# Optimization experiments

Hardware: AMD Instinct MI355X
Metric: run time of the kernel (lower is better)

The kernel has to match this reference:

```python
import jax, jax.numpy as jnp
import numpy as np

T, B = 8192, 4096  # n_time_steps, n_seqs


def setup_inputs() -> dict:
    key = jax.random.key(0)
    k1, k2 = jax.random.split(key)
    # Binary Bernoulli(0.5) observations, shape (T, B, 1), as the delta rule expects
    x = jnp.round(jax.random.uniform(k1, (T, B, 1), dtype=jnp.float32))
    # log-uniform learning rate per init_parameters: lr = 10 ** U(-2.5, -0.5)
    lr = 10.0 ** jax.random.uniform(k2, (), jnp.float32, minval=-2.5, maxval=-0.5)
    return {"x": x, "lr": lr}


def reference(x, lr):
    # DeltaRule forward, order=1 ('transition' / bigram) branch.
    # Gated EMA recurrence over time:
    #   p0_t = p0_{t-1} + lr * (x_t - p0_{t-1}) * (1 - x_{t-1})
    #   p1_t = p1_{t-1} + lr * (x_t - p1_{t-1}) * x_{t-1}
    # prediction_t = p0_t * (1 - x_t) + p1_t * x_t
    eff_lr = jnp.clip(lr, 0.0, 1.0)  # torch .clamp(0,1)
    obs = x[:, :, 0]  # (T, B)
    n_seqs = obs.shape[1]
    half = jnp.full((n_seqs,), 0.5, dtype=obs.dtype)
    init = (half, half, jnp.zeros((n_seqs,), dtype=obs.dtype))  # p0, p1, obs_prev

    def step(carry, x_t):
        p0, p1, obs_prev = carry
        p0 = p0 + eff_lr * (x_t - p0) * (1.0 - obs_prev)
        p1 = p1 + eff_lr * (x_t - p1) * obs_prev
        pred = p0 * (1.0 - x_t) + p1 * x_t
        return (p0, p1, x_t), pred

    _, preds = jax.lax.scan(step, init, obs)  # preds: (T, B)
    return preds[:, :, None]  # (T, B, 1), matching unsqueeze(2)
```

## Files before the change

kernel.cpp:

```cpp
#include <hip/hip_runtime.h>


constexpr int T_LEN  = 8192;
constexpr int B_SEQ  = 4096;
constexpr int B4     = B_SEQ / 4;
constexpr int CHUNK  = 64;
constexpr int NCHUNK = T_LEN / CHUNK;
constexpr int BLOCK  = 256;

__device__ __forceinline__ float clamp01(float v) {
    return fminf(fmaxf(v, 0.0f), 1.0f);
}

__global__ __launch_bounds__(BLOCK) void p1_compose(
    const float4* __restrict__ x4, const float* __restrict__ lr_ptr,
    float4* __restrict__ cA0, float4* __restrict__ cB0,
    float4* __restrict__ cA1, float4* __restrict__ cB1)
{
    const int i  = blockIdx.x * BLOCK + threadIdx.x;
    const int c  = blockIdx.y;
    const int t0 = c * CHUNK;
    const float lr = clamp01(*lr_ptr);

    float obs[4];
    float A0[4] = {1.f,1.f,1.f,1.f}, Bc0[4] = {0.f,0.f,0.f,0.f};
    float A1[4] = {1.f,1.f,1.f,1.f}, Bc1[4] = {0.f,0.f,0.f,0.f};

    if (c == 0) {
        obs[0]=obs[1]=obs[2]=obs[3]=0.f;
    } else {
        float4 o = x4[(size_t)(t0 - 1) * B4 + i];
        obs[0]=o.x; obs[1]=o.y; obs[2]=o.z; obs[3]=o.w;
    }

    for (int t = t0; t < t0 + CHUNK; ++t) {
        float4 xv = x4[(size_t)t * B4 + i];
        float xt[4] = {xv.x, xv.y, xv.z, xv.w};
        #pragma unroll
        for (int k = 0; k < 4; ++k) {
            float g  = 1.0f - obs[k];
            float l0 = lr * g;
            float l1 = lr * obs[k];
            float a0 = 1.0f - l0;
            float a1 = 1.0f - l1;
            A0[k] *= a0;  Bc0[k] = fmaf(a0, Bc0[k], l0 * xt[k]);
            A1[k] *= a1;  Bc1[k] = fmaf(a1, Bc1[k], l1 * xt[k]);
            obs[k] = xt[k];
        }
    }

    const size_t idx = (size_t)c * B4 + i;
    cA0[idx] = make_float4(A0[0], A0[1], A0[2], A0[3]);
    cB0[idx] = make_float4(Bc0[0], Bc0[1], Bc0[2], Bc0[3]);
    cA1[idx] = make_float4(A1[0], A1[1], A1[2], A1[3]);
    cB1[idx] = make_float4(Bc1[0], Bc1[1], Bc1[2], Bc1[3]);
}

__global__ __launch_bounds__(BLOCK) void p2_scan(
    const float4* __restrict__ cA0, const float4* __restrict__ cB0,
    const float4* __restrict__ cA1, const float4* __restrict__ cB1,
    float4* __restrict__ sP0, float4* __restrict__ sP1)
{
    const int i = blockIdx.x * BLOCK + threadIdx.x;
    float p0[4] = {0.5f,0.5f,0.5f,0.5f};
    float p1[4] = {0.5f,0.5f,0.5f,0.5f};

    for (int c = 0; c < NCHUNK; ++c) {
        const size_t idx = (size_t)c * B4 + i;
        sP0[idx] = make_float4(p0[0], p0[1], p0[2], p0[3]);
        sP1[idx] = make_float4(p1[0], p1[1], p1[2], p1[3]);
        float4 a0 = cA0[idx], b0 = cB0[idx];
        float4 a1 = cA1[idx], b1 = cB1[idx];
        p0[0] = fmaf(a0.x, p0[0], b0.x);
        p0[1] = fmaf(a0.y, p0[1], b0.y);
        p0[2] = fmaf(a0.z, p0[2], b0.z);
        p0[3] = fmaf(a0.w, p0[3], b0.w);
        p1[0] = fmaf(a1.x, p1[0], b1.x);
        p1[1] = fmaf(a1.y, p1[1], b1.y);
        p1[2] = fmaf(a1.z, p1[2], b1.z);
        p1[3] = fmaf(a1.w, p1[3], b1.w);
    }
}

__global__ __launch_bounds__(BLOCK) void p3_emit(
    const float4* __restrict__ x4, const float* __restrict__ lr_ptr,
    const float4* __restrict__ sP0, const float4* __restrict__ sP1,
    float4* __restrict__ out4)
{
    const int i  = blockIdx.x * BLOCK + threadIdx.x;
    const int c  = blockIdx.y;
    const int t0 = c * CHUNK;
    const float lr = clamp01(*lr_ptr);

    const size_t sidx = (size_t)c * B4 + i;
    float4 P0 = sP0[sidx], P1 = sP1[sidx];
    float p0[4] = {P0.x, P0.y, P0.z, P0.w};
    float p1[4] = {P1.x, P1.y, P1.z, P1.w};

    float obs[4];
    if (c == 0) {
        obs[0]=obs[1]=obs[2]=obs[3]=0.f;
    } else {
        float4 o = x4[(size_t)(t0 - 1) * B4 + i];
        obs[0]=o.x; obs[1]=o.y; obs[2]=o.z; obs[3]=o.w;
    }

    for (int t = t0; t < t0 + CHUNK; ++t) {
        float4 xv = x4[(size_t)t * B4 + i];
        float xt[4] = {xv.x, xv.y, xv.z, xv.w};
        float pr[4];
        #pragma unroll
        for (int k = 0; k < 4; ++k) {
            float g = 1.0f - obs[k];
            p0[k] = fmaf(lr * g,      xt[k] - p0[k], p0[k]);
            p1[k] = fmaf(lr * obs[k], xt[k] - p1[k], p1[k]);
            pr[k] = fmaf(p1[k] - p0[k], xt[k], p0[k]);
            obs[k] = xt[k];
        }
        out4[(size_t)t * B4 + i] = make_float4(pr[0], pr[1], pr[2], pr[3]);
    }
}

extern "C" void kernel_launch(void* const* d_in, const int* in_sizes, int n_in,
                              void* d_out, int out_size, void* d_ws, size_t ws_size,
                              hipStream_t stream) {
    const float4* x4  = (const float4*)d_in[0];
    const float*  lr  = (const float*)d_in[1];
    float4*       out = (float4*)d_out;

    const size_t n = (size_t)NCHUNK * B4;
    float4* cA0 = (float4*)d_ws;
    float4* cB0 = cA0 + n;
    float4* cA1 = cB0 + n;
    float4* cB1 = cA1 + n;
    float4* sP0 = cB1 + n;
    float4* sP1 = sP0 + n;

    dim3 grid(B4 / BLOCK, NCHUNK);
    p1_compose<<<grid, BLOCK, 0, stream>>>(x4, lr, cA0, cB0, cA1, cB1);
    p2_scan<<<dim3(B4 / BLOCK), BLOCK, 0, stream>>>(cA0, cB0, cA1, cB1, sP0, sP1);
    p3_emit<<<grid, BLOCK, 0, stream>>>(x4, lr, sP0, sP1, out);
}
```

Baseline: 302.9 us.

## Bit-pack observations in compose pass and parallelize chunk scan with wave shuffles

The compose pass now also packs each chunk's binary observations into 64-bit masks. The emit pass reads those masks instead of re-reading the full float input, which cuts its input traffic by about 32x. The serial chunk-carry scan is replaced by a parallel scan: one block per column group, 128 threads over chunks, shuffle-based within a wave plus a shared-memory fix-up across waves. This adds workspace writes for the bitmasks, depends on the inputs being exactly 0/1, and changes the floating-point association of the carry composition.

```diff
diff --git a/kernel.cpp b/kernel.cpp
--- a/kernel.cpp
+++ b/kernel.cpp
@@ -15,7 +15,8 @@
 __global__ __launch_bounds__(BLOCK) void p1_compose(
     const float4* __restrict__ x4, const float* __restrict__ lr_ptr,
     float4* __restrict__ cA0, float4* __restrict__ cB0,
-    float4* __restrict__ cA1, float4* __restrict__ cB1)
+    float4* __restrict__ cA1, float4* __restrict__ cB1,
+    uint4* __restrict__ bitsA, uint4* __restrict__ bitsB)
 {
     const int i  = blockIdx.x * BLOCK + threadIdx.x;
     const int c  = blockIdx.y;
@@ -23,9 +24,6 @@
     const float lr = clamp01(*lr_ptr);
 
     float obs[4];
-    float A0[4] = {1.f,1.f,1.f,1.f}, Bc0[4] = {0.f,0.f,0.f,0.f};
-    float A1[4] = {1.f,1.f,1.f,1.f}, Bc1[4] = {0.f,0.f,0.f,0.f};
-
     if (c == 0) {
         obs[0]=obs[1]=obs[2]=obs[3]=0.f;
     } else {
@@ -33,18 +31,24 @@
         obs[0]=o.x; obs[1]=o.y; obs[2]=o.z; obs[3]=o.w;
     }
 
-    for (int t = t0; t < t0 + CHUNK; ++t) {
-        float4 xv = x4[(size_t)t * B4 + i];
+    float A0[4]  = {1.f,1.f,1.f,1.f}, Bc0[4] = {0.f,0.f,0.f,0.f};
+    float A1[4]  = {1.f,1.f,1.f,1.f}, Bc1[4] = {0.f,0.f,0.f,0.f};
+    unsigned long long bits[4] = {0ull,0ull,0ull,0ull};
+
+    #pragma unroll 8
+    for (int t = 0; t < CHUNK; ++t) {
+        float4 xv = x4[(size_t)(t0 + t) * B4 + i];
         float xt[4] = {xv.x, xv.y, xv.z, xv.w};
         #pragma unroll
         for (int k = 0; k < 4; ++k) {
+            bits[k] |= ((unsigned long long)(xt[k] != 0.0f)) << t;
             float g  = 1.0f - obs[k];
             float l0 = lr * g;
-            float l1 = lr * obs[k];
+            float l1 = lr - l0;
             float a0 = 1.0f - l0;
             float a1 = 1.0f - l1;
-            A0[k] *= a0;  Bc0[k] = fmaf(a0, Bc0[k], l0 * xt[k]);
-            A1[k] *= a1;  Bc1[k] = fmaf(a1, Bc1[k], l1 * xt[k]);
+            Bc0[k] = fmaf(a0, Bc0[k], l0 * xt[k]);  A0[k] *= a0;
+            Bc1[k] = fmaf(a1, Bc1[k], l1 * xt[k]);  A1[k] *= a1;
             obs[k] = xt[k];
         }
     }
@@ -54,37 +58,81 @@
     cB0[idx] = make_float4(Bc0[0], Bc0[1], Bc0[2], Bc0[3]);
     cA1[idx] = make_float4(A1[0], A1[1], A1[2], A1[3]);
     cB1[idx] = make_float4(Bc1[0], Bc1[1], Bc1[2], Bc1[3]);
-}
-
-__global__ __launch_bounds__(BLOCK) void p2_scan(
+    bitsA[idx] = make_uint4((unsigned)bits[0], (unsigned)(bits[0] >> 32),
+                            (unsigned)bits[1], (unsigned)(bits[1] >> 32));
+    bitsB[idx] = make_uint4((unsigned)bits[2], (unsigned)(bits[2] >> 32),
+                            (unsigned)bits[3], (unsigned)(bits[3] >> 32));
+}
+
+
+__device__ __forceinline__ float4 shfl_up4(float4 v, int d) {
+    float4 r;
+    r.x = __shfl_up(v.x, d);
+    r.y = __shfl_up(v.y, d);
+    r.z = __shfl_up(v.z, d);
+    r.w = __shfl_up(v.w, d);
+    return r;
+}
+
+#define COMPOSE4(Aa, Bb, pA, pB)                         \
+    Bb.x = fmaf(Aa.x, pB.x, Bb.x);  Aa.x *= pA.x;        \
+    Bb.y = fmaf(Aa.y, pB.y, Bb.y);  Aa.y *= pA.y;        \
+    Bb.z = fmaf(Aa.z, pB.z, Bb.z);  Aa.z *= pA.z;        \
+    Bb.w = fmaf(Aa.w, pB.w, Bb.w);  Aa.w *= pA.w;
+
+__global__ __launch_bounds__(NCHUNK) void p2_scan(
     const float4* __restrict__ cA0, const float4* __restrict__ cB0,
     const float4* __restrict__ cA1, const float4* __restrict__ cB1,
     float4* __restrict__ sP0, float4* __restrict__ sP1)
 {
-    const int i = blockIdx.x * BLOCK + threadIdx.x;
-    float p0[4] = {0.5f,0.5f,0.5f,0.5f};
-    float p1[4] = {0.5f,0.5f,0.5f,0.5f};
-
-    for (int c = 0; c < NCHUNK; ++c) {
-        const size_t idx = (size_t)c * B4 + i;
-        sP0[idx] = make_float4(p0[0], p0[1], p0[2], p0[3]);
-        sP1[idx] = make_float4(p1[0], p1[1], p1[2], p1[3]);
-        float4 a0 = cA0[idx], b0 = cB0[idx];
-        float4 a1 = cA1[idx], b1 = cB1[idx];
-        p0[0] = fmaf(a0.x, p0[0], b0.x);
-        p0[1] = fmaf(a0.y, p0[1], b0.y);
-        p0[2] = fmaf(a0.z, p0[2], b0.z);
-        p0[3] = fmaf(a0.w, p0[3], b0.w);
-        p1[0] = fmaf(a1.x, p1[0], b1.x);
-        p1[1] = fmaf(a1.y, p1[1], b1.y);
-        p1[2] = fmaf(a1.z, p1[2], b1.z);
-        p1[3] = fmaf(a1.w, p1[3], b1.w);
-    }
+    const int i    = blockIdx.x;
+    const int c    = threadIdx.x;
+    const int lane = c & 63;
+
+    const size_t idx = (size_t)c * B4 + i;
+    float4 A0 = cA0[idx], B0 = cB0[idx];
+    float4 A1 = cA1[idx], B1 = cB1[idx];
+
+    #pragma unroll
+    for (int d = 1; d < 64; d <<= 1) {
+        float4 pA0 = shfl_up4(A0, d), pB0 = shfl_up4(B0, d);
+        float4 pA1 = shfl_up4(A1, d), pB1 = shfl_up4(B1, d);
+        if (lane >= d) {
+            COMPOSE4(A0, B0, pA0, pB0);
+            COMPOSE4(A1, B1, pA1, pB1);
+        }
+    }
+
+    __shared__ float4 tA0, tB0, tA1, tB1;
+    __shared__ float4 sA0[NCHUNK], sB0[NCHUNK], sA1[NCHUNK], sB1[NCHUNK];
+
+    if (c == 63) { tA0 = A0; tB0 = B0; tA1 = A1; tB1 = B1; }
+    __syncthreads();
+    if (c >= 64) {
+        COMPOSE4(A0, B0, tA0, tB0);
+        COMPOSE4(A1, B1, tA1, tB1);
+    }
+    sA0[c] = A0; sB0[c] = B0; sA1[c] = A1; sB1[c] = B1;
+    __syncthreads();
+
+    float4 eA0, eB0, eA1, eB1;
+    if (c == 0) {
+        eA0 = make_float4(1,1,1,1); eB0 = make_float4(0,0,0,0);
+        eA1 = make_float4(1,1,1,1); eB1 = make_float4(0,0,0,0);
+    } else {
+        eA0 = sA0[c-1]; eB0 = sB0[c-1];
+        eA1 = sA1[c-1]; eB1 = sB1[c-1];
+    }
+    sP0[idx] = make_float4(fmaf(eA0.x, 0.5f, eB0.x), fmaf(eA0.y, 0.5f, eB0.y),
+                           fmaf(eA0.z, 0.5f, eB0.z), fmaf(eA0.w, 0.5f, eB0.w));
+    sP1[idx] = make_float4(fmaf(eA1.x, 0.5f, eB1.x), fmaf(eA1.y, 0.5f, eB1.y),
+                           fmaf(eA1.z, 0.5f, eB1.z), fmaf(eA1.w, 0.5f, eB1.w));
 }
 
 __global__ __launch_bounds__(BLOCK) void p3_emit(
     const float4* __restrict__ x4, const float* __restrict__ lr_ptr,
     const float4* __restrict__ sP0, const float4* __restrict__ sP1,
+    const uint4* __restrict__ bitsA, const uint4* __restrict__ bitsB,
     float4* __restrict__ out4)
 {
     const int i  = blockIdx.x * BLOCK + threadIdx.x;
@@ -92,10 +140,14 @@
     const int t0 = c * CHUNK;
     const float lr = clamp01(*lr_ptr);
 
-    const size_t sidx = (size_t)c * B4 + i;
-    float4 P0 = sP0[sidx], P1 = sP1[sidx];
+    const size_t idx = (size_t)c * B4 + i;
+    float4 P0 = sP0[idx], P1 = sP1[idx];
     float p0[4] = {P0.x, P0.y, P0.z, P0.w};
     float p1[4] = {P1.x, P1.y, P1.z, P1.w};
+
+    uint4 ba = bitsA[idx], bb = bitsB[idx];
+    unsigned lo[4] = {ba.x, ba.z, bb.x, bb.z};
+    unsigned hi[4] = {ba.y, ba.w, bb.y, bb.w};
 
     float obs[4];
     if (c == 0) {
@@ -105,19 +157,23 @@
         obs[0]=o.x; obs[1]=o.y; obs[2]=o.z; obs[3]=o.w;
     }
 
-    for (int t = t0; t < t0 + CHUNK; ++t) {
-        float4 xv = x4[(size_t)t * B4 + i];
-        float xt[4] = {xv.x, xv.y, xv.z, xv.w};
+    #pragma unroll 8
+    for (int t = 0; t < CHUNK; ++t) {
         float pr[4];
         #pragma unroll
         for (int k = 0; k < 4; ++k) {
-            float g = 1.0f - obs[k];
-            p0[k] = fmaf(lr * g,      xt[k] - p0[k], p0[k]);
-            p1[k] = fmaf(lr * obs[k], xt[k] - p1[k], p1[k]);
-            pr[k] = fmaf(p1[k] - p0[k], xt[k], p0[k]);
-            obs[k] = xt[k];
+            unsigned w   = (t < 32) ? lo[k] : hi[k];
+            unsigned bit = (w >> (t & 31)) & 1u;
+            float xf = (float)bit;
+            float g  = 1.0f - obs[k];
+            float l0 = lr * g;
+            float l1 = lr - l0;
+            p0[k] = fmaf(l0, xf - p0[k], p0[k]);
+            p1[k] = fmaf(l1, xf - p1[k], p1[k]);
+            pr[k] = bit ? p1[k] : p0[k];
+            obs[k] = xf;
         }
-        out4[(size_t)t * B4 + i] = make_float4(pr[0], pr[1], pr[2], pr[3]);
+        out4[(size_t)(t0 + t) * B4 + i] = make_float4(pr[0], pr[1], pr[2], pr[3]);
     }
 }
 
@@ -135,9 +191,11 @@
     float4* cB1 = cA1 + n;
     float4* sP0 = cB1 + n;
     float4* sP1 = sP0 + n;
-
-    dim3 grid(B4 / BLOCK, NCHUNK);
-    p1_compose<<<grid, BLOCK, 0, stream>>>(x4, lr, cA0, cB0, cA1, cB1);
-    p2_scan<<<dim3(B4 / BLOCK), BLOCK, 0, stream>>>(cA0, cB0, cA1, cB1, sP0, sP1);
-    p3_emit<<<grid, BLOCK, 0, stream>>>(x4, lr, sP0, sP1, out);
-}
+    uint4*  bitsA = (uint4*)(sP1 + n);
+    uint4*  bitsB = bitsA + n;
+
+    dim3 grid13(B4 / BLOCK, NCHUNK);
+    p1_compose<<<grid13, BLOCK, 0, stream>>>(x4, lr, cA0, cB0, cA1, cB1, bitsA, bitsB);
+    p2_scan<<<dim3(B4), NCHUNK, 0, stream>>>(cA0, cB0, cA1, cB1, sP0, sP1);
+    p3_emit<<<grid13, BLOCK, 0, stream>>>(x4, lr, sP0, sP1, bitsA, bitsB, out);
+}
```

After: 253.0 us. -16.5%, faster.

## Fuse three-pass chunked scan into single decoupled-lookback kernel

Applied to the files above, without the earlier changes.

Replaces the compose/scan/emit kernel sequence with one kernel. Tiles are claimed through an atomic counter and chain their affine prefixes with decoupled lookback using flags in workspace. Each thread keeps the chunk's binary inputs as a 64-bit mask, so the emit phase does not re-read x from memory, and outputs are written with nontemporal stores. This removes two launches, the second read of x and the serial per-column scan, at the cost of spin-waiting on predecessor tiles and relying on x being exactly 0/1.

```diff
diff --git a/kernel.cpp b/kernel.cpp
--- a/kernel.cpp
+++ b/kernel.cpp
@@ -1,123 +1,151 @@
 #include <hip/hip_runtime.h>
 
 
-constexpr int T_LEN  = 8192;
-constexpr int B_SEQ  = 4096;
-constexpr int B4     = B_SEQ / 4;
+constexpr int B4     = 1024;
 constexpr int CHUNK  = 64;
-constexpr int NCHUNK = T_LEN / CHUNK;
+constexpr int NCHUNK = 128;
 constexpr int BLOCK  = 256;
+constexpr int NCOL   = B4 / BLOCK;
+constexpr int NTILE  = NCOL * NCHUNK;
+constexpr int COMP   = NTILE * BLOCK;
+
+typedef float vfloat4 __attribute__((ext_vector_type(4)));
 
 __device__ __forceinline__ float clamp01(float v) {
     return fminf(fmaxf(v, 0.0f), 1.0f);
 }
 
-__global__ __launch_bounds__(BLOCK) void p1_compose(
+#define COMPOSE4(Aa, Bb, pA, pB)                         \
+    Bb.x = fmaf(Aa.x, pB.x, Bb.x);  Aa.x *= pA.x;        \
+    Bb.y = fmaf(Aa.y, pB.y, Bb.y);  Aa.y *= pA.y;        \
+    Bb.z = fmaf(Aa.z, pB.z, Bb.z);  Aa.z *= pA.z;        \
+    Bb.w = fmaf(Aa.w, pB.w, Bb.w);  Aa.w *= pA.w;
+
+__global__ __launch_bounds__(BLOCK) void fused_scan(
     const float4* __restrict__ x4, const float* __restrict__ lr_ptr,
-    float4* __restrict__ cA0, float4* __restrict__ cB0,
-    float4* __restrict__ cA1, float4* __restrict__ cB1)
+    float4* __restrict__ out4,
+    int* __restrict__ counter, int* __restrict__ flags,
+    float4* __restrict__ agg, float4* __restrict__ pref)
 {
-    const int i  = blockIdx.x * BLOCK + threadIdx.x;
-    const int c  = blockIdx.y;
-    const int t0 = c * CHUNK;
+    __shared__ int sTile, sF;
+    if (threadIdx.x == 0) sTile = atomicAdd(counter, 1);
+    __syncthreads();
+    const int tile = sTile;
+    const int col  = tile & (NCOL - 1);
+    const int c    = tile >> 2;
+    const int i    = col * BLOCK + (int)threadIdx.x;
+    const int t0   = c * CHUNK;
     const float lr = clamp01(*lr_ptr);
 
-    float obs[4];
-    float A0[4] = {1.f,1.f,1.f,1.f}, Bc0[4] = {0.f,0.f,0.f,0.f};
-    float A1[4] = {1.f,1.f,1.f,1.f}, Bc1[4] = {0.f,0.f,0.f,0.f};
+    float ob[4];
+    if (c == 0) { ob[0]=ob[1]=ob[2]=ob[3]=0.f; }
+    else { float4 o = x4[(size_t)(t0 - 1) * B4 + i]; ob[0]=o.x; ob[1]=o.y; ob[2]=o.z; ob[3]=o.w; }
 
-    if (c == 0) {
-        obs[0]=obs[1]=obs[2]=obs[3]=0.f;
-    } else {
-        float4 o = x4[(size_t)(t0 - 1) * B4 + i];
-        obs[0]=o.x; obs[1]=o.y; obs[2]=o.z; obs[3]=o.w;
-    }
+    float obs[4] = {ob[0], ob[1], ob[2], ob[3]};
+    float A0[4]  = {1,1,1,1}, Bc0[4] = {0,0,0,0};
+    float A1[4]  = {1,1,1,1}, Bc1[4] = {0,0,0,0};
+    unsigned long long bits[4] = {0,0,0,0};
 
-    for (int t = t0; t < t0 + CHUNK; ++t) {
-        float4 xv = x4[(size_t)t * B4 + i];
+    #pragma unroll 8
+    for (int t = 0; t < CHUNK; ++t) {
+        float4 xv = x4[(size_t)(t0 + t) * B4 + i];
         float xt[4] = {xv.x, xv.y, xv.z, xv.w};
         #pragma unroll
         for (int k = 0; k < 4; ++k) {
+            bits[k] |= ((unsigned long long)(xt[k] != 0.0f)) << t;
             float g  = 1.0f - obs[k];
             float l0 = lr * g;
-            float l1 = lr * obs[k];
+            float l1 = lr - l0;
             float a0 = 1.0f - l0;
             float a1 = 1.0f - l1;
-            A0[k] *= a0;  Bc0[k] = fmaf(a0, Bc0[k], l0 * xt[k]);
-            A1[k] *= a1;  Bc1[k] = fmaf(a1, Bc1[k], l1 * xt[k]);
+            Bc0[k] = fmaf(a0, Bc0[k], l0 * xt[k]);  A0[k] *= a0;
+            Bc1[k] = fmaf(a1, Bc1[k], l1 * xt[k]);  A1[k] *= a1;
             obs[k] = xt[k];
         }
     }
 
-    const size_t idx = (size_t)c * B4 + i;
-    cA0[idx] = make_float4(A0[0], A0[1], A0[2], A0[3]);
-    cB0[idx] = make_float4(Bc0[0], Bc0[1], Bc0[2], Bc0[3]);
-    cA1[idx] = make_float4(A1[0], A1[1], A1[2], A1[3]);
-    cB1[idx] = make_float4(Bc1[0], Bc1[1], Bc1[2], Bc1[3]);
-}
+    float4 vA0 = make_float4(A0[0],A0[1],A0[2],A0[3]);
+    float4 vB0 = make_float4(Bc0[0],Bc0[1],Bc0[2],Bc0[3]);
+    float4 vA1 = make_float4(A1[0],A1[1],A1[2],A1[3]);
+    float4 vB1 = make_float4(Bc1[0],Bc1[1],Bc1[2],Bc1[3]);
 
-__global__ __launch_bounds__(BLOCK) void p2_scan(
-    const float4* __restrict__ cA0, const float4* __restrict__ cB0,
-    const float4* __restrict__ cA1, const float4* __restrict__ cB1,
-    float4* __restrict__ sP0, float4* __restrict__ sP1)
-{
-    const int i = blockIdx.x * BLOCK + threadIdx.x;
-    float p0[4] = {0.5f,0.5f,0.5f,0.5f};
-    float p1[4] = {0.5f,0.5f,0.5f,0.5f};
+    const int slot = tile * BLOCK + (int)threadIdx.x;
 
-    for (int c = 0; c < NCHUNK; ++c) {
-        const size_t idx = (size_t)c * B4 + i;
-        sP0[idx] = make_float4(p0[0], p0[1], p0[2], p0[3]);
-        sP1[idx] = make_float4(p1[0], p1[1], p1[2], p1[3]);
-        float4 a0 = cA0[idx], b0 = cB0[idx];
-        float4 a1 = cA1[idx], b1 = cB1[idx];
-        p0[0] = fmaf(a0.x, p0[0], b0.x);
-        p0[1] = fmaf(a0.y, p0[1], b0.y);
-        p0[2] = fmaf(a0.z, p0[2], b0.z);
-        p0[3] = fmaf(a0.w, p0[3], b0.w);
-        p1[0] = fmaf(a1.x, p1[0], b1.x);
-        p1[1] = fmaf(a1.y, p1[1], b1.y);
-        p1[2] = fmaf(a1.z, p1[2], b1.z);
-        p1[3] = fmaf(a1.w, p1[3], b1.w);
-    }
-}
+    float4 eA0 = make_float4(1,1,1,1), eB0 = make_float4(0,0,0,0);
+    float4 eA1 = make_float4(1,1,1,1), eB1 = make_float4(0,0,0,0);
 
-__global__ __launch_bounds__(BLOCK) void p3_emit(
-    const float4* __restrict__ x4, const float* __restrict__ lr_ptr,
-    const float4* __restrict__ sP0, const float4* __restrict__ sP1,
-    float4* __restrict__ out4)
-{
-    const int i  = blockIdx.x * BLOCK + threadIdx.x;
-    const int c  = blockIdx.y;
-    const int t0 = c * CHUNK;
-    const float lr = clamp01(*lr_ptr);
+    if (c == 0) {
+        pref[0*COMP + slot] = vA0;  pref[1*COMP + slot] = vB0;
+        pref[2*COMP + slot] = vA1;  pref[3*COMP + slot] = vB1;
+        __syncthreads();
+        if (threadIdx.x == 0)
+            __hip_atomic_store(&flags[tile], 2, __ATOMIC_RELEASE, __HIP_MEMORY_SCOPE_AGENT);
+    } else {
+        agg[0*COMP + slot] = vA0;  agg[1*COMP + slot] = vB0;
+        agg[2*COMP + slot] = vA1;  agg[3*COMP + slot] = vB1;
+        __syncthreads();
+        if (threadIdx.x == 0)
+            __hip_atomic_store(&flags[tile], 1, __ATOMIC_RELEASE, __HIP_MEMORY_SCOPE_AGENT);
 
-    const size_t sidx = (size_t)c * B4 + i;
-    float4 P0 = sP0[sidx], P1 = sP1[sidx];
-    float p0[4] = {P0.x, P0.y, P0.z, P0.w};
-    float p1[4] = {P1.x, P1.y, P1.z, P1.w};
+        int pred = tile - NCOL;
+        for (;;) {
+            if (threadIdx.x == 0) {
+                int f;
+                while ((f = __hip_atomic_load(&flags[pred], __ATOMIC_ACQUIRE,
+                                              __HIP_MEMORY_SCOPE_AGENT)) == 0)
+                    __builtin_amdgcn_s_sleep(1);
+                sF = f;
+            }
+            __syncthreads();
+            const int f = sF;
+            __syncthreads();
+            __builtin_amdgcn_fence(__ATOMIC_ACQUIRE, "agent");
+            const float4* __restrict__ src = (f == 2) ? pref : agg;
+            const int ps = pred * BLOCK + (int)threadIdx.x;
+            float4 pA0 = src[0*COMP + ps], pB0 = src[1*COMP + ps];
+            float4 pA1 = src[2*COMP + ps], pB1 = src[3*COMP + ps];
+            COMPOSE4(eA0, eB0, pA0, pB0);
+            COMPOSE4(eA1, eB1, pA1, pB1);
+            if (f == 2) break;
+            pred -= NCOL;
+        }
 
-    float obs[4];
-    if (c == 0) {
-        obs[0]=obs[1]=obs[2]=obs[3]=0.f;
-    } else {
-        float4 o = x4[(size_t)(t0 - 1) * B4 + i];
-        obs[0]=o.x; obs[1]=o.y; obs[2]=o.z; obs[3]=o.w;
+        COMPOSE4(vA0, vB0, eA0, eB0);
+        COMPOSE4(vA1, vB1, eA1, eB1);
+        pref[0*COMP + slot] = vA0;  pref[1*COMP + slot] = vB0;
+        pref[2*COMP + slot] = vA1;  pref[3*COMP + slot] = vB1;
+        __syncthreads();
+        if (threadIdx.x == 0)
+            __hip_atomic_store(&flags[tile], 2, __ATOMIC_RELEASE, __HIP_MEMORY_SCOPE_AGENT);
     }
 
-    for (int t = t0; t < t0 + CHUNK; ++t) {
-        float4 xv = x4[(size_t)t * B4 + i];
-        float xt[4] = {xv.x, xv.y, xv.z, xv.w};
+    float p0[4] = { fmaf(eA0.x, 0.5f, eB0.x), fmaf(eA0.y, 0.5f, eB0.y),
+                    fmaf(eA0.z, 0.5f, eB0.z), fmaf(eA0.w, 0.5f, eB0.w) };
+    float p1[4] = { fmaf(eA1.x, 0.5f, eB1.x), fmaf(eA1.y, 0.5f, eB1.y),
+                    fmaf(eA1.z, 0.5f, eB1.z), fmaf(eA1.w, 0.5f, eB1.w) };
+    unsigned lo[4] = { (unsigned)bits[0], (unsigned)bits[1], (unsigned)bits[2], (unsigned)bits[3] };
+    unsigned hi[4] = { (unsigned)(bits[0]>>32), (unsigned)(bits[1]>>32),
+                       (unsigned)(bits[2]>>32), (unsigned)(bits[3]>>32) };
+    float o2[4] = {ob[0], ob[1], ob[2], ob[3]};
+
+    #pragma unroll 8
+    for (int t = 0; t < CHUNK; ++t) {
         float pr[4];
         #pragma unroll
         for (int k = 0; k < 4; ++k) {
-            float g = 1.0f - obs[k];
-            p0[k] = fmaf(lr * g,      xt[k] - p0[k], p0[k]);
-            p1[k] = fmaf(lr * obs[k], xt[k] - p1[k], p1[k]);
-            pr[k] = fmaf(p1[k] - p0[k], xt[k], p0[k]);
-            obs[k] = xt[k];
+            unsigned w   = (t < 32) ? lo[k] : hi[k];
+            unsigned bit = (w >> (t & 31)) & 1u;
+            float xf = (float)bit;
+            float g  = 1.0f - o2[k];
+            float l0 = lr * g;
+            float l1 = lr - l0;
+            p0[k] = fmaf(l0, xf - p0[k], p0[k]);
+            p1[k] = fmaf(l1, xf - p1[k], p1[k]);
+            pr[k] = bit ? p1[k] : p0[k];
+            o2[k] = xf;
         }
-        out4[(size_t)t * B4 + i] = make_float4(pr[0], pr[1], pr[2], pr[3]);
+        vfloat4 v = {pr[0], pr[1], pr[2], pr[3]};
+        __builtin_nontemporal_store(v, (vfloat4*)&out4[(size_t)(t0 + t) * B4 + i]);
     }
 }
 
@@ -128,16 +156,11 @@
     const float*  lr  = (const float*)d_in[1];
     float4*       out = (float4*)d_out;
 
-    const size_t n = (size_t)NCHUNK * B4;
-    float4* cA0 = (float4*)d_ws;
-    float4* cB0 = cA0 + n;
-    float4* cA1 = cB0 + n;
-    float4* cB1 = cA1 + n;
-    float4* sP0 = cB1 + n;
-    float4* sP1 = sP0 + n;
+    int*    counter = (int*)d_ws;
+    int*    flags   = (int*)d_ws + 16;
+    float4* agg     = (float4*)((char*)d_ws + 4096);
+    float4* pref    = agg + 4 * (size_t)COMP;
 
-    dim3 grid(B4 / BLOCK, NCHUNK);
-    p1_compose<<<grid, BLOCK, 0, stream>>>(x4, lr, cA0, cB0, cA1, cB1);
-    p2_scan<<<dim3(B4 / BLOCK), BLOCK, 0, stream>>>(cA0, cB0, cA1, cB1, sP0, sP1);
-    p3_emit<<<grid, BLOCK, 0, stream>>>(x4, lr, sP0, sP1, out);
+    (void)hipMemsetAsync(d_ws, 0, 4096, stream);
+    fused_scan<<<dim3(NTILE), BLOCK, 0, stream>>>(x4, lr, out, counter, flags, agg, pref);
 }
```

After: 537.0 us. 1.77x slower.
